# Optimization experiments

Hardware: AMD Instinct MI355X
Metric: run time of the kernel (lower is better)

Reference implementation:

```python
import jax, jax.numpy as jnp
import numpy as np

N, E, F = 50000, 1600000, 128
H1, C1 = 8, 16   # conv1: heads=8, out=16 -> concat 128
H2, C2 = 1, 16   # conv2: heads=1, out=num_classes=16


def _gat_conv(x, edge_index, W, a_src, a_dst, b, heads, out_ch):
    """PyG GATConv with self-loops, additive attention, dst-segmented softmax."""
    n = x.shape[0]
    loop = jnp.arange(n, dtype=edge_index.dtype)
    src = jnp.concatenate([edge_index[0], loop])  # [Et]
    dst = jnp.concatenate([edge_index[1], loop])  # [Et]
    h = (x @ W).reshape(n, heads, out_ch)                      # [N,H,C]
    alpha_s = jnp.sum(h * a_src[None], axis=-1)                # [N,H]
    alpha_d = jnp.sum(h * a_dst[None], axis=-1)                # [N,H]
    e = jax.nn.leaky_relu(alpha_s[src] + alpha_d[dst], 0.2)    # [Et,H]
    # segment softmax over destination node (self-loops guarantee nonempty segments)
    m = jax.lax.stop_gradient(jax.ops.segment_max(e, dst, num_segments=n))
    ex = jnp.exp(e - m[dst])
    denom = jax.ops.segment_sum(ex, dst, num_segments=n)
    alpha = ex / denom[dst]                                    # [Et,H]
    msg = h[src] * alpha[:, :, None]                           # [Et,H,C]
    out = jax.ops.segment_sum(msg, dst, num_segments=n)        # [N,H,C]
    return out.reshape(n, heads * out_ch) + b


def setup_inputs() -> dict:
    key = jax.random.key(0)
    ks = jax.random.split(key, 10)
    sc = 0.1
    x = jax.random.normal(ks[0], (N, F), dtype=jnp.float32)
    edge_index = jax.random.randint(ks[1], (2, E), 0, N, dtype=jnp.int32)
    return {
        "x": x,
        "edge_index": edge_index,
        "W1": jax.random.normal(ks[2], (F, H1 * C1), dtype=jnp.float32) * sc,
        "a_src1": jax.random.normal(ks[3], (H1, C1), dtype=jnp.float32) * sc,
        "a_dst1": jax.random.normal(ks[4], (H1, C1), dtype=jnp.float32) * sc,
        "b1": jnp.zeros((H1 * C1,), dtype=jnp.float32),
        "W2": jax.random.normal(ks[5], (H1 * C1, H2 * C2), dtype=jnp.float32) * sc,
        "a_src2": jax.random.normal(ks[6], (H2, C2), dtype=jnp.float32) * sc,
        "a_dst2": jax.random.normal(ks[7], (H2, C2), dtype=jnp.float32) * sc,
        "b2": jnp.zeros((H2 * C2,), dtype=jnp.float32),
    }


def reference(x, edge_index, W1, a_src1, a_dst1, b1, W2, a_src2, a_dst2, b2):
    h = _gat_conv(x, edge_index, W1, a_src1, a_dst1, b1, H1, C1)
    h = jax.nn.elu(h)
    # dropout p=0.6 is identity in eval mode
    return _gat_conv(h, edge_index, W2, a_src2, a_dst2, b2, H2, C2)
```

## Files before the change

### kernel.cpp

```cpp
#include <hip/hip_runtime.h>
#include <hip/hip_bf16.h>

#define NN 50000
#define NE 1600000
#define ET (NE + NN)
#define H1 8
#define C1 16
#define D1 128
#define C2 16
#define NB1 196
#define OCTW 6250
#define NSL 64
#define SLE (NE / NSL)

#define HIST_NB 512
#define PACK_NB 1563
#define PREP_NB 8
#define SCAT_NB 512
#define GEMM_NB 782

typedef unsigned short u16;
typedef unsigned int u32;
typedef u32 u32x4 __attribute__((ext_vector_type(4)));
typedef __bf16 bf16x8 __attribute__((ext_vector_type(8)));
typedef float f32x4v __attribute__((ext_vector_type(4)));

__device__ void hist_role(int hbid, char* smem, const int* __restrict__ ei,
                          u16* __restrict__ hs) {
  int* hl = (int*)smem;
  const int oct = hbid & 7;
  const int s   = hbid >> 3;
  const int lo  = oct * OCTW;
  const int tid = threadIdx.x;
  for (int j = tid; j < OCTW; j += 256) hl[j] = 0;
  __syncthreads();
  const int4* dp = (const int4*)(ei + NE) + (size_t)s * (SLE / 4);
  for (int g = tid; g < SLE / 4; g += 256) {
    int4 v = dp[g];
    int a = v.x - lo, b = v.y - lo, c = v.z - lo, d = v.w - lo;
    if ((unsigned)a < OCTW) atomicAdd(&hl[a], 1);
    if ((unsigned)b < OCTW) atomicAdd(&hl[b], 1);
    if ((unsigned)c < OCTW) atomicAdd(&hl[c], 1);
    if ((unsigned)d < OCTW) atomicAdd(&hl[d], 1);
  }
  __syncthreads();
  u16* out = hs + (size_t)s * NN + lo;
  for (int j = tid; j < OCTW; j += 256) out[j] = (u16)hl[j];
}

__device__ void pack_role(int pbid, const int* __restrict__ ei,
                          u16* __restrict__ src16, u16* __restrict__ dst16) {
  int i = pbid * 256 + threadIdx.x;
  if (i >= NE / 4) return;
  int4 s = ((const int4*)ei)[i];
  int4 d = ((const int4*)(ei + NE))[i];
  ushort4 sp; sp.x = (u16)s.x; sp.y = (u16)s.y; sp.z = (u16)s.z; sp.w = (u16)s.w;
  ushort4 dp; dp.x = (u16)d.x; dp.y = (u16)d.y; dp.z = (u16)d.z; dp.w = (u16)d.w;
  ((ushort4*)src16)[i] = sp;
  ((ushort4*)dst16)[i] = dp;
}

__device__ void prep_role(int pbid, const float* __restrict__ W1,
    const float* __restrict__ aS, const float* __restrict__ aD,
    __hip_bfloat16* __restrict__ WextT) {
  const int k = threadIdx.x;
  if (k >= 128) return;
  const int h = pbid;
#pragma unroll
  for (int j = 0; j < 16; ++j) {
    int n = h * 16 + j;
    WextT[(size_t)n * 128 + k] = __float2bfloat16(W1[(size_t)k * 128 + n]);
  }
  float s = 0.f, dv = 0.f;
#pragma unroll
  for (int c = 0; c < 16; ++c) {
    float w = W1[(size_t)k * 128 + h * 16 + c];
    s  = fmaf(w, aS[h * 16 + c], s);
    dv = fmaf(w, aD[h * 16 + c], dv);
  }
  WextT[(size_t)(128 + h) * 128 + k] = __float2bfloat16(s);
  WextT[(size_t)(136 + h) * 128 + k] = __float2bfloat16(dv);
}

__global__ __launch_bounds__(256) void k1_fused(const int* __restrict__ ei,
    u16* __restrict__ hs, u16* __restrict__ src16, u16* __restrict__ dst16,
    const float* __restrict__ W1, const float* __restrict__ aS,
    const float* __restrict__ aD, __hip_bfloat16* __restrict__ WextT) {
  __shared__ __align__(16) char smem[25088];
  const int bid = blockIdx.x;
  if (bid < HIST_NB) hist_role(bid, smem, ei, hs);
  else if (bid < HIST_NB + PACK_NB) pack_role(bid - HIST_NB, ei, src16, dst16);
  else prep_role(bid - HIST_NB - PACK_NB, W1, aS, aD, WextT);
}

__global__ __launch_bounds__(256) void scan1_k(u16* __restrict__ hs,
                                               int* __restrict__ deg32,
                                               int* __restrict__ incl,
                                               int* __restrict__ bsum) {
  __shared__ int sm[256];
  int t = threadIdx.x, i = blockIdx.x * 256 + t;
  int v = 0;
  if (i < NN) {
    int run = 0;
#pragma unroll
    for (int s = 0; s < NSL; ++s) {
      int c = (int)hs[(size_t)s * NN + i];
      hs[(size_t)s * NN + i] = (u16)run;
      run += c;
    }
    v = run + 1;
    deg32[i] = v;
  }
  sm[t] = v; __syncthreads();
  for (int off = 1; off < 256; off <<= 1) {
    int u = (t >= off) ? sm[t - off] : 0;
    __syncthreads();
    sm[t] += u;
    __syncthreads();
  }
  if (i < NN) incl[i] = sm[t];
  if (t == 255) bsum[blockIdx.x] = sm[255];
}

__global__ __launch_bounds__(256) void scan2_k(const int* __restrict__ bsum, int* __restrict__ boff) {
  __shared__ int sm[256];
  int t = threadIdx.x;
  int v = (t < NB1) ? bsum[t] : 0;
  sm[t] = v; __syncthreads();
  for (int off = 1; off < 256; off <<= 1) {
    int u = (t >= off) ? sm[t - off] : 0;
    __syncthreads();
    sm[t] += u;
    __syncthreads();
  }
  if (t < NB1) boff[t] = sm[t] - v;
}

__global__ __launch_bounds__(256) void scan3_k(const int* __restrict__ deg32,
                                               const int* __restrict__ incl,
                                               const int* __restrict__ boff,
                                               int* __restrict__ rowptr,
                                               u16* __restrict__ srcs) {
  int i = blockIdx.x * 256 + threadIdx.x;
  if (i >= NN) return;
  int dg = deg32[i];
  int r = incl[i] - dg + boff[i >> 8];
  rowptr[i] = r;
  srcs[r + dg - 1] = (u16)i;
  if (i == 0) rowptr[NN] = ET;
}

__device__ void scatter_role(int sbid, char* smem, const u16* __restrict__ src16,
    const u16* __restrict__ dst16, const int* __restrict__ rowptr,
    const u16* __restrict__ hs, u16* __restrict__ srcs) {
  int* cur = (int*)smem;
  const int oct = sbid & 7;
  const int s   = sbid >> 3;
  const int lo  = oct * OCTW;
  const int tid = threadIdx.x;
  const u16* seed = hs + (size_t)s * NN + lo;
  for (int j = tid; j < OCTW; j += 256)
    cur[j] = rowptr[lo + j] + (int)seed[j];
  __syncthreads();
  const u32x4* dp = (const u32x4*)dst16 + (size_t)s * (SLE / 8);
  const u32x4* sp = (const u32x4*)src16 + (size_t)s * (SLE / 8);
  for (int g = tid; g < SLE / 8; g += 256) {
    u32x4 dv = __builtin_nontemporal_load(&dp[g]);
    u32x4 sv = __builtin_nontemporal_load(&sp[g]);
#pragma unroll
    for (int q = 0; q < 4; ++q) {
      int d0 = (int)(dv[q] & 0xffffu) - lo;
      int d1 = (int)(dv[q] >> 16) - lo;
      if ((unsigned)d0 < OCTW) srcs[atomicAdd(&cur[d0], 1)] = (u16)(sv[q] & 0xffffu);
      if ((unsigned)d1 < OCTW) srcs[atomicAdd(&cur[d1], 1)] = (u16)(sv[q] >> 16);
    }
  }
}

__device__ void gemm1_role(int bid, const float* __restrict__ X,
    const __hip_bfloat16* __restrict__ WextT,
    __hip_bfloat16* __restrict__ Yb, float* __restrict__ as1, float* __restrict__ ad1) {
  const int tid = threadIdx.x;
  const int wv = tid >> 6, lane = tid & 63;
  const int row0 = bid * 64 + wv * 16;
  const int mrow = lane & 15;
  const int kq = lane >> 4;
  int garow = row0 + mrow; if (garow > NN - 1) garow = NN - 1;
  const float* xrow = X + (size_t)garow * D1 + kq * 8;
  const char* bbase = (const char*)WextT + (size_t)mrow * 256 + kq * 16;
  f32x4v acc[9] = {};
#pragma unroll
  for (int kt = 0; kt < 4; ++kt) {
    float4 xa = *(const float4*)(xrow + kt * 32);
    float4 xb = *(const float4*)(xrow + kt * 32 + 4);
    bf16x8 af;
    af[0] = (__bf16)xa.x; af[1] = (__bf16)xa.y; af[2] = (__bf16)xa.z; af[3] = (__bf16)xa.w;
    af[4] = (__bf16)xb.x; af[5] = (__bf16)xb.y; af[6] = (__bf16)xb.z; af[7] = (__bf16)xb.w;
#pragma unroll
    for (int nt = 0; nt < 9; ++nt) {
      u32x4 braw = *(const u32x4*)(bbase + (size_t)nt * 4096 + kt * 64);
      bf16x8 bfr = __builtin_bit_cast(bf16x8, braw);
      acc[nt] = __builtin_amdgcn_mfma_f32_16x16x32_bf16(af, bfr, acc[nt], 0, 0, 0);
    }
  }
  const int cl = lane & 15;
#pragma unroll
  for (int reg = 0; reg < 4; ++reg) {
    int gr = row0 + (lane >> 4) * 4 + reg;
    if (gr < NN) {
#pragma unroll
      for (int nt = 0; nt < 8; ++nt)
        Yb[(size_t)gr * D1 + nt * 16 + cl] = __float2bfloat16(acc[nt][reg]);
      float lv = acc[8][reg];
      if (cl < 8) as1[gr * H1 + cl] = lv;
      else        ad1[gr * H1 + (cl - 8)] = lv;
    }
  }
}

__global__ __launch_bounds__(256) void k2_fused(const u16* __restrict__ src16,
    const u16* __restrict__ dst16, const int* __restrict__ rowptr,
    const u16* __restrict__ hs, u16* __restrict__ srcs,
    const float* __restrict__ X, const __hip_bfloat16* __restrict__ WextT,
    __hip_bfloat16* __restrict__ Yb, float* __restrict__ as1, float* __restrict__ ad1) {
  __shared__ __align__(16) char smem[25088];
  const int bid = blockIdx.x;
  if (bid < SCAT_NB) scatter_role(bid, smem, src16, dst16, rowptr, hs, srcs);
  else gemm1_role(bid - SCAT_NB, X, WextT, Yb, as1, ad1);
}

__global__ __launch_bounds__(128) void agg1_k(const int* __restrict__ rowptr,
    const u16* __restrict__ srcs, const u32* __restrict__ h1u,
    const float* __restrict__ as, const float* __restrict__ ad,
    const float* __restrict__ b, u32* __restrict__ zb) {
  __shared__ int ssrc[2][64];
  __shared__ float wl[2][64 * 9];
  __shared__ int lens[2];
  const int w = threadIdx.x >> 6;
  const int lane = threadIdx.x & 63;
  const int d = blockIdx.x * 2 + w;
  const int h = lane >> 3;
  const int beg = rowptr[d], end = rowptr[d + 1];
  if (lane == 0) lens[w] = end - beg;
  __syncthreads();
  const int nb = (max(lens[0], lens[1]) + 63) >> 6;
  const float4 adv0 = *(const float4*)(ad + (size_t)d * H1);
  const float4 adv1 = *(const float4*)(ad + (size_t)d * H1 + 4);
  float aL0 = 0, aL1 = 0, aL2 = 0, aL3 = 0;
  float aH0 = 0, aH1 = 0, aH2 = 0, aH3 = 0;
  float dn0 = 0, dn1 = 0, dn2 = 0, dn3 = 0;
  for (int it = 0; it < nb; ++it) {
    const int base = beg + (it << 6);
    int m = end - base; m = m < 0 ? 0 : (m > 64 ? 64 : m);
    if (lane < m) {
      int s = (int)srcs[base + lane];
      ssrc[w][lane] = s;
      const float4 a0 = *(const float4*)(as + (size_t)s * H1);
      const float4 a1 = *(const float4*)(as + (size_t)s * H1 + 4);
      float* wp = &wl[w][lane * 9];
      float e;
      e = a0.x + adv0.x; e = e > 0.f ? e : 0.2f * e; wp[0] = __expf(e);
      e = a0.y + adv0.y; e = e > 0.f ? e : 0.2f * e; wp[1] = __expf(e);
      e = a0.z + adv0.z; e = e > 0.f ? e : 0.2f * e; wp[2] = __expf(e);
      e = a0.w + adv0.w; e = e > 0.f ? e : 0.2f * e; wp[3] = __expf(e);
      e = a1.x + adv1.x; e = e > 0.f ? e : 0.2f * e; wp[4] = __expf(e);
      e = a1.y + adv1.y; e = e > 0.f ? e : 0.2f * e; wp[5] = __expf(e);
      e = a1.z + adv1.z; e = e > 0.f ? e : 0.2f * e; wp[6] = __expf(e);
      e = a1.w + adv1.w; e = e > 0.f ? e : 0.2f * e; wp[7] = __expf(e);
    }
    __syncthreads();
    int j = 0;
    for (; j + 4 <= m; j += 4) {
      int s0 = ssrc[w][j], s1 = ssrc[w][j + 1], s2 = ssrc[w][j + 2], s3 = ssrc[w][j + 3];
      float w0 = wl[w][(j + 0) * 9 + h], w1 = wl[w][(j + 1) * 9 + h];
      float w2 = wl[w][(j + 2) * 9 + h], w3 = wl[w][(j + 3) * 9 + h];
      u32 v0 = h1u[(size_t)s0 * 64 + lane];
      u32 v1 = h1u[(size_t)s1 * 64 + lane];
      u32 v2 = h1u[(size_t)s2 * 64 + lane];
      u32 v3 = h1u[(size_t)s3 * 64 + lane];
      dn0 += w0; dn1 += w1; dn2 += w2; dn3 += w3;
      aL0 = fmaf(w0, __uint_as_float(v0 << 16), aL0);
      aH0 = fmaf(w0, __uint_as_float(v0 & 0xffff0000u), aH0);
      aL1 = fmaf(w1, __uint_as_float(v1 << 16), aL1);
      aH1 = fmaf(w1, __uint_as_float(v1 & 0xffff0000u), aH1);
      aL2 = fmaf(w2, __uint_as_float(v2 << 16), aL2);
      aH2 = fmaf(w2, __uint_as_float(v2 & 0xffff0000u), aH2);
      aL3 = fmaf(w3, __uint_as_float(v3 << 16), aL3);
      aH3 = fmaf(w3, __uint_as_float(v3 & 0xffff0000u), aH3);
    }
    for (; j < m; ++j) {
      int s0 = ssrc[w][j];
      float w0 = wl[w][j * 9 + h];
      u32 v0 = h1u[(size_t)s0 * 64 + lane];
      dn0 += w0;
      aL0 = fmaf(w0, __uint_as_float(v0 << 16), aL0);
      aH0 = fmaf(w0, __uint_as_float(v0 & 0xffff0000u), aH0);
    }
    __syncthreads();
  }
  float den = (dn0 + dn1) + (dn2 + dn3);
  float aL = (aL0 + aL1) + (aL2 + aL3);
  float aH = (aH0 + aH1) + (aH2 + aH3);
  float inv = 1.f / den;
  float2 bb = *(const float2*)(b + lane * 2);
  float v0 = aL * inv + bb.x;
  float v1 = aH * inv + bb.y;
  v0 = v0 > 0.f ? v0 : __expf(v0) - 1.f;
  v1 = v1 > 0.f ? v1 : __expf(v1) - 1.f;
  __hip_bfloat16 z0 = __float2bfloat16(v0), z1 = __float2bfloat16(v1);
  u32 pu = ((u32)(*(u16*)&z1) << 16) | (u32)(*(u16*)&z0);
  zb[(size_t)d * 64 + lane] = pu;
}

__global__ __launch_bounds__(256) void gemm2_k(const u32* __restrict__ Zb,
    const float* __restrict__ W, const float* __restrict__ aS,
    const float* __restrict__ aD, __hip_bfloat16* __restrict__ Yb,
    float* __restrict__ as2, float* __restrict__ ad2) {
  __shared__ float Ws[D1][C2];
  __shared__ float Zs[16][D1 + 4];
  const int tid = threadIdx.x;
  for (int i = tid; i < D1 * C2; i += 256) Ws[i >> 4][i & 15] = W[i];
  const int rb = blockIdx.x * 16;
  {
    int r = tid >> 4, c8 = tid & 15;
    u32x4 raw = *(const u32x4*)(Zb + (size_t)(rb + r) * 64 + c8 * 4);
    float* dst = &Zs[r][c8 * 8];
#pragma unroll
    for (int q = 0; q < 4; ++q) {
      dst[2 * q]     = __uint_as_float(raw[q] << 16);
      dst[2 * q + 1] = __uint_as_float(raw[q] & 0xffff0000u);
    }
  }
  __syncthreads();
  const int r = tid >> 4, c = tid & 15;
  float a0 = 0, a1 = 0, a2 = 0, a3 = 0;
#pragma unroll
  for (int k = 0; k < D1; k += 4) {
    float4 z4 = *(const float4*)&Zs[r][k];
    a0 = fmaf(z4.x, Ws[k][c], a0);
    a1 = fmaf(z4.y, Ws[k + 1][c], a1);
    a2 = fmaf(z4.z, Ws[k + 2][c], a2);
    a3 = fmaf(z4.w, Ws[k + 3][c], a3);
  }
  float acc = (a0 + a1) + (a2 + a3);
  Yb[(size_t)(rb + r) * C2 + c] = __float2bfloat16(acc);
  float ps = acc * aS[c], pd = acc * aD[c];
  ps += __shfl_xor(ps, 1); pd += __shfl_xor(pd, 1);
  ps += __shfl_xor(ps, 2); pd += __shfl_xor(pd, 2);
  ps += __shfl_xor(ps, 4); pd += __shfl_xor(pd, 4);
  ps += __shfl_xor(ps, 8); pd += __shfl_xor(pd, 8);
  if (c == 0) { as2[rb + r] = ps; ad2[rb + r] = pd; }
}

__global__ __launch_bounds__(256) void agg2_k(const int* __restrict__ rowptr,
    const u16* __restrict__ srcs, const u32* __restrict__ h2u,
    const float* __restrict__ as, const float* __restrict__ ad,
    const float* __restrict__ b, float* __restrict__ outp) {
  const int wv = threadIdx.x >> 6;
  const int lane = threadIdx.x & 63;
  const int d = blockIdx.x * 4 + wv;
  const int j8 = lane >> 3, cp = lane & 7;
  const int beg = rowptr[d], end = rowptr[d + 1];
  const float adv = ad[d];
  float a0 = 0, a1 = 0, den = 0;
  for (int base = beg; base < end; base += 64) {
    const int m = end - base;
    float wreg = 0.f; int sreg = 0;
    if (lane < m) {
      sreg = (int)srcs[base + lane];
      float e = as[sreg] + adv;
      e = e > 0.f ? e : 0.2f * e;
      wreg = __expf(e);
    }
    const int mm = m < 64 ? m : 64;
    const int rounds = (mm + 7) >> 3;
    for (int r = 0; r < rounds; ++r) {
      int src_lane = r * 8 + j8;
      float wgt = __shfl(wreg, src_lane);
      int s     = __shfl(sreg, src_lane);
      if (wgt > 0.f) {
        u32 v = h2u[(size_t)s * 8 + cp];
        den += wgt;
        a0 = fmaf(wgt, __uint_as_float(v << 16), a0);
        a1 = fmaf(wgt, __uint_as_float(v & 0xffff0000u), a1);
      }
    }
  }
#pragma unroll
  for (int off = 8; off < 64; off <<= 1) {
    a0 += __shfl_xor(a0, off);
    a1 += __shfl_xor(a1, off);
    den += __shfl_xor(den, off);
  }
  if (j8 == 0) {
    float inv = 1.f / den;
    float2 bb = *(const float2*)(b + cp * 2);
    float2 o = {a0 * inv + bb.x, a1 * inv + bb.y};
    *(float2*)(outp + (size_t)d * C2 + cp * 2) = o;
  }
}

extern "C" void kernel_launch(void* const* d_in, const int* in_sizes, int n_in,
                              void* d_out, int out_size, void* d_ws, size_t ws_size,
                              hipStream_t stream) {
  const float* x    = (const float*)d_in[0];
  const int*   ei   = (const int*)d_in[1];
  const float* W1   = (const float*)d_in[2];
  const float* aS1  = (const float*)d_in[3];
  const float* aD1  = (const float*)d_in[4];
  const float* b1   = (const float*)d_in[5];
  const float* W2   = (const float*)d_in[6];
  const float* aS2  = (const float*)d_in[7];
  const float* aD2  = (const float*)d_in[8];
  const float* b2   = (const float*)d_in[9];
  float* outp = (float*)d_out;

  char* p = (char*)d_ws;
  __hip_bfloat16* h1b = (__hip_bfloat16*)p; p += (size_t)NN * D1 * 2;
  u32* zb   = (u32*)p; p += (size_t)NN * 64 * 4;
  float* as1  = (float*)p; p += (size_t)NN * H1 * 4;
  float* ad1  = (float*)p; p += (size_t)NN * H1 * 4;
  __hip_bfloat16* WextT = (__hip_bfloat16*)p; p += (size_t)144 * 128 * 2;
  u16*   hs     = (u16*)p; p += (size_t)NSL * NN * 2;
  int*   deg32  = (int*)p; p += (size_t)NN * 4;
  int*   incl   = (int*)p; p += (size_t)NN * 4;
  int*   rowptr = (int*)p; p += (size_t)(NN + 1) * 4;
  int*   bsum   = (int*)p; p += 256 * 4;
  int*   boff   = (int*)p; p += 256 * 4;
  u16*   srcs   = (u16*)p; p += (size_t)ET * 2;
  u16*   src16  = (u16*)p; p += (size_t)NE * 2;
  u16*   dst16  = (u16*)p; p += (size_t)NE * 2;
  __hip_bfloat16* h2b = h1b;
  float* as2 = (float*)(h1b + (size_t)NN * C2);
  float* ad2 = as2 + NN;

  k1_fused<<<HIST_NB + PACK_NB + PREP_NB, 256, 0, stream>>>(
      ei, hs, src16, dst16, W1, aS1, aD1, WextT);

  scan1_k<<<NB1, 256, 0, stream>>>(hs, deg32, incl, bsum);
  scan2_k<<<1, 256, 0, stream>>>(bsum, boff);
  scan3_k<<<NB1, 256, 0, stream>>>(deg32, incl, boff, rowptr, srcs);

  k2_fused<<<SCAT_NB + GEMM_NB, 256, 0, stream>>>(
      src16, dst16, rowptr, hs, srcs, x, WextT, h1b, as1, ad1);

  agg1_k <<<NN / 2, 128, 0, stream>>>(rowptr, srcs, (const u32*)h1b, as1, ad1, b1, zb);

  gemm2_k<<<NN / 16, 256, 0, stream>>>(zb, W2, aS2, aD2, h2b, as2, ad2);
  agg2_k <<<NN / 4, 256, 0, stream>>>(rowptr, srcs, (const u32*)h2b, as2, ad2, b2, outp);
}
```

Measured before the change: 255.4 us.

## Fuse layer-2 GEMM into agg1, merge scan kernels, double histogram slices

Folds the second GAT linear transform and its attention projections into the epilogue of the first aggregation kernel. Each wave reduces its 16 outputs with cross-lane shuffles, so the bf16 intermediate z buffer and the separate gemm2 launch are no longer needed. The block-offset scan is merged into scan3, with every block redundantly scanning the block sums, which removes one launch. Histogram and scatter slices double from 64 to 128 and the scatter loads drop to 8-byte vectors, raising parallelism at the cost of a larger per-slice histogram buffer and more per-node scan work. Index arithmetic also moves to 32-bit shifts, and the 64-step shuffle reduction adds ALU work to every agg1 wave.

```diff
diff --git a/kernel.cpp b/kernel.cpp
--- a/kernel.cpp
+++ b/kernel.cpp
@@ -5,23 +5,23 @@
 #define NE 1600000
 #define ET (NE + NN)
 #define H1 8
-#define C1 16
 #define D1 128
 #define C2 16
 #define NB1 196
 #define OCTW 6250
-#define NSL 64
+#define NSL 128
 #define SLE (NE / NSL)
 
-#define HIST_NB 512
+#define HIST_NB 1024
 #define PACK_NB 1563
 #define PREP_NB 8
-#define SCAT_NB 512
+#define SCAT_NB 1024
 #define GEMM_NB 782
 
 typedef unsigned short u16;
 typedef unsigned int u32;
 typedef u32 u32x4 __attribute__((ext_vector_type(4)));
+typedef u32 u32x2 __attribute__((ext_vector_type(2)));
 typedef __bf16 bf16x8 __attribute__((ext_vector_type(8)));
 typedef float f32x4v __attribute__((ext_vector_type(4)));
 
@@ -102,7 +102,7 @@
   int v = 0;
   if (i < NN) {
     int run = 0;
-#pragma unroll
+#pragma unroll 16
     for (int s = 0; s < NSL; ++s) {
       int c = (int)hs[(size_t)s * NN + i];
       hs[(size_t)s * NN + i] = (u16)run;
@@ -122,9 +122,13 @@
   if (t == 255) bsum[blockIdx.x] = sm[255];
 }
 
-__global__ __launch_bounds__(256) void scan2_k(const int* __restrict__ bsum, int* __restrict__ boff) {
+__global__ __launch_bounds__(256) void scan3_k(const int* __restrict__ deg32,
+                                               const int* __restrict__ incl,
+                                               const int* __restrict__ bsum,
+                                               int* __restrict__ rowptr,
+                                               u16* __restrict__ srcs) {
   __shared__ int sm[256];
-  int t = threadIdx.x;
+  const int t = threadIdx.x, b = blockIdx.x;
   int v = (t < NB1) ? bsum[t] : 0;
   sm[t] = v; __syncthreads();
   for (int off = 1; off < 256; off <<= 1) {
@@ -133,18 +137,11 @@
     sm[t] += u;
     __syncthreads();
   }
-  if (t < NB1) boff[t] = sm[t] - v;
-}
-
-__global__ __launch_bounds__(256) void scan3_k(const int* __restrict__ deg32,
-                                               const int* __restrict__ incl,
-                                               const int* __restrict__ boff,
-                                               int* __restrict__ rowptr,
-                                               u16* __restrict__ srcs) {
-  int i = blockIdx.x * 256 + threadIdx.x;
+  const int boff = (b == 0) ? 0 : sm[b - 1];
+  int i = b * 256 + t;
   if (i >= NN) return;
   int dg = deg32[i];
-  int r = incl[i] - dg + boff[i >> 8];
+  int r = incl[i] - dg + boff;
   rowptr[i] = r;
   srcs[r + dg - 1] = (u16)i;
   if (i == 0) rowptr[NN] = ET;
@@ -162,18 +159,19 @@
   for (int j = tid; j < OCTW; j += 256)
     cur[j] = rowptr[lo + j] + (int)seed[j];
   __syncthreads();
-  const u32x4* dp = (const u32x4*)dst16 + (size_t)s * (SLE / 8);
-  const u32x4* sp = (const u32x4*)src16 + (size_t)s * (SLE / 8);
-  for (int g = tid; g < SLE / 8; g += 256) {
-    u32x4 dv = __builtin_nontemporal_load(&dp[g]);
-    u32x4 sv = __builtin_nontemporal_load(&sp[g]);
-#pragma unroll
-    for (int q = 0; q < 4; ++q) {
-      int d0 = (int)(dv[q] & 0xffffu) - lo;
-      int d1 = (int)(dv[q] >> 16) - lo;
-      if ((unsigned)d0 < OCTW) srcs[atomicAdd(&cur[d0], 1)] = (u16)(sv[q] & 0xffffu);
-      if ((unsigned)d1 < OCTW) srcs[atomicAdd(&cur[d1], 1)] = (u16)(sv[q] >> 16);
-    }
+  const u32x2* dp = (const u32x2*)dst16 + (size_t)s * (SLE / 4);
+  const u32x2* sp = (const u32x2*)src16 + (size_t)s * (SLE / 4);
+  for (int g = tid; g < SLE / 4; g += 256) {
+    u32x2 dv = __builtin_nontemporal_load(&dp[g]);
+    u32x2 sv = __builtin_nontemporal_load(&sp[g]);
+    int d0 = (int)(dv.x & 0xffffu) - lo;
+    int d1 = (int)(dv.x >> 16) - lo;
+    int d2 = (int)(dv.y & 0xffffu) - lo;
+    int d3 = (int)(dv.y >> 16) - lo;
+    if ((unsigned)d0 < OCTW) srcs[atomicAdd(&cur[d0], 1)] = (u16)(sv.x & 0xffffu);
+    if ((unsigned)d1 < OCTW) srcs[atomicAdd(&cur[d1], 1)] = (u16)(sv.x >> 16);
+    if ((unsigned)d2 < OCTW) srcs[atomicAdd(&cur[d2], 1)] = (u16)(sv.y & 0xffffu);
+    if ((unsigned)d3 < OCTW) srcs[atomicAdd(&cur[d3], 1)] = (u16)(sv.y >> 16);
   }
 }
 
@@ -232,7 +230,9 @@
 __global__ __launch_bounds__(128) void agg1_k(const int* __restrict__ rowptr,
     const u16* __restrict__ srcs, const u32* __restrict__ h1u,
     const float* __restrict__ as, const float* __restrict__ ad,
-    const float* __restrict__ b, u32* __restrict__ zb) {
+    const float* __restrict__ b, const float* __restrict__ W2,
+    const float* __restrict__ aS2, const float* __restrict__ aD2,
+    u32* __restrict__ h2u_out, float* __restrict__ as2, float* __restrict__ ad2) {
   __shared__ int ssrc[2][64];
   __shared__ float wl[2][64 * 9];
   __shared__ int lens[2];
@@ -244,8 +244,8 @@
   if (lane == 0) lens[w] = end - beg;
   __syncthreads();
   const int nb = (max(lens[0], lens[1]) + 63) >> 6;
-  const float4 adv0 = *(const float4*)(ad + (size_t)d * H1);
-  const float4 adv1 = *(const float4*)(ad + (size_t)d * H1 + 4);
+  const float4 adv0 = *(const float4*)(ad + ((u32)d << 3));
+  const float4 adv1 = *(const float4*)(ad + ((u32)d << 3) + 4);
   float aL0 = 0, aL1 = 0, aL2 = 0, aL3 = 0;
   float aH0 = 0, aH1 = 0, aH2 = 0, aH3 = 0;
   float dn0 = 0, dn1 = 0, dn2 = 0, dn3 = 0;
@@ -255,8 +255,8 @@
     if (lane < m) {
       int s = (int)srcs[base + lane];
       ssrc[w][lane] = s;
-      const float4 a0 = *(const float4*)(as + (size_t)s * H1);
-      const float4 a1 = *(const float4*)(as + (size_t)s * H1 + 4);
+      const float4 a0 = *(const float4*)(as + ((u32)s << 3));
+      const float4 a1 = *(const float4*)(as + ((u32)s << 3) + 4);
       float* wp = &wl[w][lane * 9];
       float e;
       e = a0.x + adv0.x; e = e > 0.f ? e : 0.2f * e; wp[0] = __expf(e);
@@ -274,10 +274,10 @@
       int s0 = ssrc[w][j], s1 = ssrc[w][j + 1], s2 = ssrc[w][j + 2], s3 = ssrc[w][j + 3];
       float w0 = wl[w][(j + 0) * 9 + h], w1 = wl[w][(j + 1) * 9 + h];
       float w2 = wl[w][(j + 2) * 9 + h], w3 = wl[w][(j + 3) * 9 + h];
-      u32 v0 = h1u[(size_t)s0 * 64 + lane];
-      u32 v1 = h1u[(size_t)s1 * 64 + lane];
-      u32 v2 = h1u[(size_t)s2 * 64 + lane];
-      u32 v3 = h1u[(size_t)s3 * 64 + lane];
+      u32 v0 = h1u[((u32)s0 << 6) | lane];
+      u32 v1 = h1u[((u32)s1 << 6) | lane];
+      u32 v2 = h1u[((u32)s2 << 6) | lane];
+      u32 v3 = h1u[((u32)s3 << 6) | lane];
       dn0 += w0; dn1 += w1; dn2 += w2; dn3 += w3;
       aL0 = fmaf(w0, __uint_as_float(v0 << 16), aL0);
       aH0 = fmaf(w0, __uint_as_float(v0 & 0xffff0000u), aH0);
@@ -291,7 +291,7 @@
     for (; j < m; ++j) {
       int s0 = ssrc[w][j];
       float w0 = wl[w][j * 9 + h];
-      u32 v0 = h1u[(size_t)s0 * 64 + lane];
+      u32 v0 = h1u[((u32)s0 << 6) | lane];
       dn0 += w0;
       aL0 = fmaf(w0, __uint_as_float(v0 << 16), aL0);
       aH0 = fmaf(w0, __uint_as_float(v0 & 0xffff0000u), aH0);
@@ -307,49 +307,31 @@
   float v1 = aH * inv + bb.y;
   v0 = v0 > 0.f ? v0 : __expf(v0) - 1.f;
   v1 = v1 > 0.f ? v1 : __expf(v1) - 1.f;
-  __hip_bfloat16 z0 = __float2bfloat16(v0), z1 = __float2bfloat16(v1);
-  u32 pu = ((u32)(*(u16*)&z1) << 16) | (u32)(*(u16*)&z0);
-  zb[(size_t)d * 64 + lane] = pu;
-}
-
-__global__ __launch_bounds__(256) void gemm2_k(const u32* __restrict__ Zb,
-    const float* __restrict__ W, const float* __restrict__ aS,
-    const float* __restrict__ aD, __hip_bfloat16* __restrict__ Yb,
-    float* __restrict__ as2, float* __restrict__ ad2) {
-  __shared__ float Ws[D1][C2];
-  __shared__ float Zs[16][D1 + 4];
-  const int tid = threadIdx.x;
-  for (int i = tid; i < D1 * C2; i += 256) Ws[i >> 4][i & 15] = W[i];
-  const int rb = blockIdx.x * 16;
-  {
-    int r = tid >> 4, c8 = tid & 15;
-    u32x4 raw = *(const u32x4*)(Zb + (size_t)(rb + r) * 64 + c8 * 4);
-    float* dst = &Zs[r][c8 * 8];
-#pragma unroll
-    for (int q = 0; q < 4; ++q) {
-      dst[2 * q]     = __uint_as_float(raw[q] << 16);
-      dst[2 * q + 1] = __uint_as_float(raw[q] & 0xffff0000u);
-    }
-  }
-  __syncthreads();
-  const int r = tid >> 4, c = tid & 15;
-  float a0 = 0, a1 = 0, a2 = 0, a3 = 0;
-#pragma unroll
-  for (int k = 0; k < D1; k += 4) {
-    float4 z4 = *(const float4*)&Zs[r][k];
-    a0 = fmaf(z4.x, Ws[k][c], a0);
-    a1 = fmaf(z4.y, Ws[k + 1][c], a1);
-    a2 = fmaf(z4.z, Ws[k + 2][c], a2);
-    a3 = fmaf(z4.w, Ws[k + 3][c], a3);
-  }
-  float acc = (a0 + a1) + (a2 + a3);
-  Yb[(size_t)(rb + r) * C2 + c] = __float2bfloat16(acc);
-  float ps = acc * aS[c], pd = acc * aD[c];
-  ps += __shfl_xor(ps, 1); pd += __shfl_xor(pd, 1);
-  ps += __shfl_xor(ps, 2); pd += __shfl_xor(pd, 2);
-  ps += __shfl_xor(ps, 4); pd += __shfl_xor(pd, 4);
-  ps += __shfl_xor(ps, 8); pd += __shfl_xor(pd, 8);
-  if (c == 0) { as2[rb + r] = ps; ad2[rb + r] = pd; }
+  const float4* w2r0 = (const float4*)(W2 + (u32)(lane * 2) * 16);
+  const float4* w2r1 = (const float4*)(W2 + (u32)(lane * 2 + 1) * 16);
+  float p[16];
+#pragma unroll
+  for (int q = 0; q < 4; ++q) {
+    float4 wa = w2r0[q], wb = w2r1[q];
+    p[4 * q + 0] = v0 * wa.x + v1 * wb.x;
+    p[4 * q + 1] = v0 * wa.y + v1 * wb.y;
+    p[4 * q + 2] = v0 * wa.z + v1 * wb.z;
+    p[4 * q + 3] = v0 * wa.w + v1 * wb.w;
+  }
+#pragma unroll
+  for (int off = 1; off < 64; off <<= 1) {
+#pragma unroll
+    for (int c = 0; c < 16; ++c) p[c] += __shfl_xor(p[c], off);
+  }
+  float ps = 0.f, pd = 0.f;
+#pragma unroll
+  for (int c = 0; c < 16; ++c) { ps = fmaf(p[c], aS2[c], ps); pd = fmaf(p[c], aD2[c], pd); }
+  if (lane == 0) { as2[d] = ps; ad2[d] = pd; }
+  if (lane < 8) {
+    __hip_bfloat16 e0 = __float2bfloat16(p[2 * lane]);
+    __hip_bfloat16 e1 = __float2bfloat16(p[2 * lane + 1]);
+    h2u_out[((u32)d << 3) | lane] = ((u32)(*(u16*)&e1) << 16) | (u32)(*(u16*)&e0);
+  }
 }
 
 __global__ __launch_bounds__(256) void agg2_k(const int* __restrict__ rowptr,
@@ -379,7 +361,7 @@
       float wgt = __shfl(wreg, src_lane);
       int s     = __shfl(sreg, src_lane);
       if (wgt > 0.f) {
-        u32 v = h2u[(size_t)s * 8 + cp];
+        u32 v = h2u[((u32)s << 3) | cp];
         den += wgt;
         a0 = fmaf(wgt, __uint_as_float(v << 16), a0);
         a1 = fmaf(wgt, __uint_as_float(v & 0xffff0000u), a1);
@@ -417,35 +399,32 @@
 
   char* p = (char*)d_ws;
   __hip_bfloat16* h1b = (__hip_bfloat16*)p; p += (size_t)NN * D1 * 2;
-  u32* zb   = (u32*)p; p += (size_t)NN * 64 * 4;
   float* as1  = (float*)p; p += (size_t)NN * H1 * 4;
   float* ad1  = (float*)p; p += (size_t)NN * H1 * 4;
+  u32*   h2u  = (u32*)p;  p += (size_t)NN * 8 * 4;
+  float* as2  = (float*)p; p += (size_t)NN * 4;
+  float* ad2  = (float*)p; p += (size_t)NN * 4;
   __hip_bfloat16* WextT = (__hip_bfloat16*)p; p += (size_t)144 * 128 * 2;
   u16*   hs     = (u16*)p; p += (size_t)NSL * NN * 2;
   int*   deg32  = (int*)p; p += (size_t)NN * 4;
   int*   incl   = (int*)p; p += (size_t)NN * 4;
   int*   rowptr = (int*)p; p += (size_t)(NN + 1) * 4;
   int*   bsum   = (int*)p; p += 256 * 4;
-  int*   boff   = (int*)p; p += 256 * 4;
   u16*   srcs   = (u16*)p; p += (size_t)ET * 2;
   u16*   src16  = (u16*)p; p += (size_t)NE * 2;
   u16*   dst16  = (u16*)p; p += (size_t)NE * 2;
-  __hip_bfloat16* h2b = h1b;
-  float* as2 = (float*)(h1b + (size_t)NN * C2);
-  float* ad2 = as2 + NN;
 
   k1_fused<<<HIST_NB + PACK_NB + PREP_NB, 256, 0, stream>>>(
       ei, hs, src16, dst16, W1, aS1, aD1, WextT);
 
   scan1_k<<<NB1, 256, 0, stream>>>(hs, deg32, incl, bsum);
-  scan2_k<<<1, 256, 0, stream>>>(bsum, boff);
-  scan3_k<<<NB1, 256, 0, stream>>>(deg32, incl, boff, rowptr, srcs);
+  scan3_k<<<NB1, 256, 0, stream>>>(deg32, incl, bsum, rowptr, srcs);
 
   k2_fused<<<SCAT_NB + GEMM_NB, 256, 0, stream>>>(
       src16, dst16, rowptr, hs, srcs, x, WextT, h1b, as1, ad1);
 
-  agg1_k <<<NN / 2, 128, 0, stream>>>(rowptr, srcs, (const u32*)h1b, as1, ad1, b1, zb);
-
-  gemm2_k<<<NN / 16, 256, 0, stream>>>(zb, W2, aS2, aD2, h2b, as2, ad2);
-  agg2_k <<<NN / 4, 256, 0, stream>>>(rowptr, srcs, (const u32*)h2b, as2, ad2, b2, outp);
-}
+  agg1_k<<<NN / 2, 128, 0, stream>>>(rowptr, srcs, (const u32*)h1b, as1, ad1,
+                                     b1, W2, aS2, aD2, h2u, as2, ad2);
+
+  agg2_k<<<NN / 4, 256, 0, stream>>>(rowptr, srcs, h2u, as2, ad2, b2, outp);
+}
```

Measured after the change: 272.5 us. 6.7% more time.
